# Optimization experiments

Measured on AMD Instinct MI355X. Metric: run time of the kernel, lower is better.

## Reference

```python
import jax, jax.numpy as jnp
import numpy as np

N = 8192          # number of nodes
E = 524288        # number of edges (avg degree 64)
D = 256           # latent_dim
NEG_FILL = -1e9   # torch.full fill value


def setup_inputs() -> dict:
    key = jax.random.key(0)
    k1, k2, k3, k4, k5, k6 = jax.random.split(key, 6)
    encoded = jax.random.normal(k1, (N, D), dtype=jnp.float32)
    h = jax.random.normal(k2, (N, D), dtype=jnp.float32)
    edge_index = jax.random.randint(k3, (2, E), 0, N, dtype=jnp.int64)
    edge_attr = jax.random.normal(k4, (E,), dtype=jnp.float32)
    # Linear weights (bias=False); stored as [in, out] for x @ W
    W1 = jax.random.normal(k5, (2 * D + 1, D), dtype=jnp.float32) * (1.0 / np.sqrt(2 * D + 1))
    W2 = jax.random.normal(k6, (D, 1), dtype=jnp.float32) * (1.0 / np.sqrt(D))
    return {"encoded": encoded, "h": h, "edge_index": edge_index,
            "edge_attr": edge_attr, "W1": W1, "W2": W2}


def reference(encoded, h, edge_index, edge_attr, W1, W2):
    left, right = edge_index[0], edge_index[1]
    # gather endpoint states and concat with scalar edge feature -> [E, 2D+1]
    feats = jnp.concatenate([h[left], h[right], edge_attr[:, None]], axis=1)
    # 2-layer MLP (no bias): Linear -> ReLU -> Linear -> [E]
    scores = (jax.nn.relu(feats @ W1) @ W2)[:, 0]
    # scatter into dense (N, N) matrix prefilled with -1e9
    result = jnp.full((h.shape[0], h.shape[0]), NEG_FILL, dtype=h.dtype)
    return result.at[left, right].set(scores)
```

## Files before the change

kernel.cpp:

```cpp
#include <hip/hip_runtime.h>

#define N_NODES 8192
#define E_EDGES 524288
#define D_DIM   256
#define NEG_FILL -1e9f

#define PROJ_BLOCKS 256
#define ROWS_PER_BLOCK 32
#define FILL_BLOCKS 1792

#define EDGE_BLOCKS 2048
#define EDGES_PER_WAVE 64

typedef float vfloat4 __attribute__((ext_vector_type(4)));
typedef float vfloat2 __attribute__((ext_vector_type(2)));

__global__ __launch_bounds__(256) void fill_proj_kernel(
    const float* __restrict__ h,
    const float* __restrict__ W1,
    float* __restrict__ out,
    unsigned char* __restrict__ AB)
{
    if (blockIdx.x < PROJ_BLOCKS) {
        __shared__ float hs[ROWS_PER_BLOCK * D_DIM];
        const int t  = threadIdx.x;
        const int r0 = blockIdx.x * ROWS_PER_BLOCK;
        const float* hp = h + (long long)r0 * D_DIM;
        for (int i = t; i < ROWS_PER_BLOCK * D_DIM; i += 256) hs[i] = hp[i];
        __syncthreads();

        float accA[ROWS_PER_BLOCK];
        float accB[ROWS_PER_BLOCK];
        #pragma unroll
        for (int r = 0; r < ROWS_PER_BLOCK; ++r) { accA[r] = 0.f; accB[r] = 0.f; }

        for (int k = 0; k < D_DIM; k += 4) {
            float wa0 = W1[(k + 0) * D_DIM + t];
            float wa1 = W1[(k + 1) * D_DIM + t];
            float wa2 = W1[(k + 2) * D_DIM + t];
            float wa3 = W1[(k + 3) * D_DIM + t];
            float wb0 = W1[(256 + k + 0) * D_DIM + t];
            float wb1 = W1[(256 + k + 1) * D_DIM + t];
            float wb2 = W1[(256 + k + 2) * D_DIM + t];
            float wb3 = W1[(256 + k + 3) * D_DIM + t];
            #pragma unroll
            for (int r = 0; r < ROWS_PER_BLOCK; ++r) {
                const float4 hv = *(const float4*)&hs[r * D_DIM + k];
                accA[r] = fmaf(hv.x, wa0, accA[r]);
                accA[r] = fmaf(hv.y, wa1, accA[r]);
                accA[r] = fmaf(hv.z, wa2, accA[r]);
                accA[r] = fmaf(hv.w, wa3, accA[r]);
                accB[r] = fmaf(hv.x, wb0, accB[r]);
                accB[r] = fmaf(hv.y, wb1, accB[r]);
                accB[r] = fmaf(hv.z, wb2, accB[r]);
                accB[r] = fmaf(hv.w, wb3, accB[r]);
            }
        }

        unsigned char* A = AB;
        unsigned char* B = AB + (long long)N_NODES * D_DIM;
        #pragma unroll
        for (int r = 0; r < ROWS_PER_BLOCK; ++r) {
            int pa = __builtin_amdgcn_cvt_pk_fp8_f32(accA[r], accA[r], 0, false);
            int pb = __builtin_amdgcn_cvt_pk_fp8_f32(accB[r], accB[r], 0, false);
            A[(long long)(r0 + r) * D_DIM + t] = (unsigned char)(pa & 0xFF);
            B[(long long)(r0 + r) * D_DIM + t] = (unsigned char)(pb & 0xFF);
        }
    } else {
        const int b = blockIdx.x - PROJ_BLOCKS;
        const int nvec = (N_NODES / 4) * N_NODES;
        vfloat4 fv = { NEG_FILL, NEG_FILL, NEG_FILL, NEG_FILL };
        vfloat4* o4 = (vfloat4*)out;
        for (int i = b * 256 + threadIdx.x; i < nvec; i += FILL_BLOCKS * 256)
            __builtin_nontemporal_store(fv, &o4[i]);
    }
}

__global__ __launch_bounds__(256) void edge_kernel(
    const int* __restrict__ eidx,
    const float* __restrict__ eattr,
    const float* __restrict__ W1,
    const float* __restrict__ W2,
    const unsigned char* __restrict__ AB,
    float* __restrict__ out)
{
    const int wave = blockIdx.x * 4 + (threadIdx.x >> 6);
    const int lane = threadIdx.x & 63;
    const int g    = lane >> 4;
    const int t    = lane & 15;
    const int base = wave * EDGES_PER_WAVE;

    const int   l_all = eidx[base + lane];
    const int   r_all = eidx[E_EDGES + base + lane];
    const float a_all = eattr[base + lane];

    const int j0 = t * 16;
    const float4 wl0 = *(const float4*)&W1[512 * D_DIM + j0 + 0];
    const float4 wl1 = *(const float4*)&W1[512 * D_DIM + j0 + 4];
    const float4 wl2 = *(const float4*)&W1[512 * D_DIM + j0 + 8];
    const float4 wl3 = *(const float4*)&W1[512 * D_DIM + j0 + 12];
    const float4 w20 = *(const float4*)&W2[j0 + 0];
    const float4 w21 = *(const float4*)&W2[j0 + 4];
    const float4 w22 = *(const float4*)&W2[j0 + 8];
    const float4 w23 = *(const float4*)&W2[j0 + 12];
    const unsigned char* Bt = AB + (long long)N_NODES * D_DIM;

    int   l_c  = __shfl(l_all, g);
    int   r_c  = __shfl(r_all, g);
    float at_c = __shfl(a_all, g);
    uint4 av_c = *(const uint4*)(AB + (unsigned)l_c * D_DIM + j0);
    uint4 bv_c = *(const uint4*)(Bt + (unsigned)r_c * D_DIM + j0);

    #pragma unroll 4
    for (int i = 0; i < EDGES_PER_WAVE / 4; ++i) {
        const int   l_cur = l_c;
        const int   r_cur = r_c;
        const float attr  = at_c;
        const uint4 av    = av_c;
        const uint4 bv    = bv_c;
        if (i + 1 < EDGES_PER_WAVE / 4) {
            l_c  = __shfl(l_all, 4 * (i + 1) + g);
            r_c  = __shfl(r_all, 4 * (i + 1) + g);
            at_c = __shfl(a_all, 4 * (i + 1) + g);
            av_c = *(const uint4*)(AB + (unsigned)l_c * D_DIM + j0);
            bv_c = *(const uint4*)(Bt + (unsigned)r_c * D_DIM + j0);
        }

        float s = 0.f;
        #define MLP_STEP(AV, BV, WL, W2V) {                                        \
            vfloat2 alo = __builtin_amdgcn_cvt_pk_f32_fp8((int)(AV), false);       \
            vfloat2 ahi = __builtin_amdgcn_cvt_pk_f32_fp8((int)(AV), true);        \
            vfloat2 blo = __builtin_amdgcn_cvt_pk_f32_fp8((int)(BV), false);       \
            vfloat2 bhi = __builtin_amdgcn_cvt_pk_f32_fp8((int)(BV), true);        \
            float hv;                                                              \
            hv = fmaf(attr, WL.x, alo.x + blo.x); hv = fmaxf(hv, 0.f); s = fmaf(hv, W2V.x, s); \
            hv = fmaf(attr, WL.y, alo.y + blo.y); hv = fmaxf(hv, 0.f); s = fmaf(hv, W2V.y, s); \
            hv = fmaf(attr, WL.z, ahi.x + bhi.x); hv = fmaxf(hv, 0.f); s = fmaf(hv, W2V.z, s); \
            hv = fmaf(attr, WL.w, ahi.y + bhi.y); hv = fmaxf(hv, 0.f); s = fmaf(hv, W2V.w, s); \
        }
        MLP_STEP(av.x, bv.x, wl0, w20);
        MLP_STEP(av.y, bv.y, wl1, w21);
        MLP_STEP(av.z, bv.z, wl2, w22);
        MLP_STEP(av.w, bv.w, wl3, w23);
        #undef MLP_STEP

        s += __shfl_xor(s, 8);
        s += __shfl_xor(s, 4);
        s += __shfl_xor(s, 2);
        s += __shfl_xor(s, 1);

        if (t == 0)
            __builtin_nontemporal_store(
                s, &out[(long long)l_cur * N_NODES + r_cur]);
    }
}

extern "C" void kernel_launch(void* const* d_in, const int* in_sizes, int n_in,
                              void* d_out, int out_size, void* d_ws, size_t ws_size,
                              hipStream_t stream) {
    const float* h     = (const float*)d_in[1];
    const int*   eidx  = (const int*)d_in[2];
    const float* eattr = (const float*)d_in[3];
    const float* W1    = (const float*)d_in[4];
    const float* W2    = (const float*)d_in[5];
    float* out = (float*)d_out;
    unsigned char* AB = (unsigned char*)d_ws;

    fill_proj_kernel<<<PROJ_BLOCKS + FILL_BLOCKS, 256, 0, stream>>>(h, W1, out, AB);
    edge_kernel<<<EDGE_BLOCKS, 256, 0, stream>>>(eidx, eattr, W1, W2, AB, out);
}
```

Baseline: 387.3 us.

## Pack edge indices, vectorize edge MLP with packed float2, drop LDS staging

```diff
diff --git a/kernel.cpp b/kernel.cpp
--- a/kernel.cpp
+++ b/kernel.cpp
@@ -22,12 +22,8 @@
     unsigned char* __restrict__ AB)
 {
     if (blockIdx.x < PROJ_BLOCKS) {
-        __shared__ float hs[ROWS_PER_BLOCK * D_DIM];
         const int t  = threadIdx.x;
         const int r0 = blockIdx.x * ROWS_PER_BLOCK;
-        const float* hp = h + (long long)r0 * D_DIM;
-        for (int i = t; i < ROWS_PER_BLOCK * D_DIM; i += 256) hs[i] = hp[i];
-        __syncthreads();
 
         float accA[ROWS_PER_BLOCK];
         float accB[ROWS_PER_BLOCK];
@@ -45,7 +41,7 @@
             float wb3 = W1[(256 + k + 3) * D_DIM + t];
             #pragma unroll
             for (int r = 0; r < ROWS_PER_BLOCK; ++r) {
-                const float4 hv = *(const float4*)&hs[r * D_DIM + k];
+                const float4 hv = *(const float4*)&h[(r0 + r) * D_DIM + k];
                 accA[r] = fmaf(hv.x, wa0, accA[r]);
                 accA[r] = fmaf(hv.y, wa1, accA[r]);
                 accA[r] = fmaf(hv.z, wa2, accA[r]);
@@ -90,68 +86,66 @@
     const int t    = lane & 15;
     const int base = wave * EDGES_PER_WAVE;
 
-    const int   l_all = eidx[base + lane];
-    const int   r_all = eidx[E_EDGES + base + lane];
-    const float a_all = eattr[base + lane];
+    const int   l_all = __builtin_nontemporal_load(&eidx[base + lane]);
+    const int   r_all = __builtin_nontemporal_load(&eidx[E_EDGES + base + lane]);
+    const float a_all = __builtin_nontemporal_load(&eattr[base + lane]);
+    const int   lr_all = (l_all << 13) | r_all;
 
     const int j0 = t * 16;
-    const float4 wl0 = *(const float4*)&W1[512 * D_DIM + j0 + 0];
-    const float4 wl1 = *(const float4*)&W1[512 * D_DIM + j0 + 4];
-    const float4 wl2 = *(const float4*)&W1[512 * D_DIM + j0 + 8];
-    const float4 wl3 = *(const float4*)&W1[512 * D_DIM + j0 + 12];
-    const float4 w20 = *(const float4*)&W2[j0 + 0];
-    const float4 w21 = *(const float4*)&W2[j0 + 4];
-    const float4 w22 = *(const float4*)&W2[j0 + 8];
-    const float4 w23 = *(const float4*)&W2[j0 + 12];
+    vfloat2 wl[8], w2[8];
+    const vfloat2* wlp = (const vfloat2*)&W1[512 * D_DIM + j0];
+    const vfloat2* w2p = (const vfloat2*)&W2[j0];
+    #pragma unroll
+    for (int i = 0; i < 8; ++i) { wl[i] = wlp[i]; w2[i] = w2p[i]; }
     const unsigned char* Bt = AB + (long long)N_NODES * D_DIM;
+    const vfloat2 zero2 = { 0.f, 0.f };
 
-    int   l_c  = __shfl(l_all, g);
-    int   r_c  = __shfl(r_all, g);
+    int   lr_c = __shfl(lr_all, g);
     float at_c = __shfl(a_all, g);
-    uint4 av_c = *(const uint4*)(AB + (unsigned)l_c * D_DIM + j0);
-    uint4 bv_c = *(const uint4*)(Bt + (unsigned)r_c * D_DIM + j0);
+    uint4 av_c = *(const uint4*)(AB + (unsigned)(lr_c >> 13) * D_DIM + j0);
+    uint4 bv_c = *(const uint4*)(Bt + (unsigned)(lr_c & 8191) * D_DIM + j0);
 
     #pragma unroll 4
     for (int i = 0; i < EDGES_PER_WAVE / 4; ++i) {
-        const int   l_cur = l_c;
-        const int   r_cur = r_c;
-        const float attr  = at_c;
-        const uint4 av    = av_c;
-        const uint4 bv    = bv_c;
+        const int   lr_cur = lr_c;
+        const float attr   = at_c;
+        const uint4 av     = av_c;
+        const uint4 bv     = bv_c;
         if (i + 1 < EDGES_PER_WAVE / 4) {
-            l_c  = __shfl(l_all, 4 * (i + 1) + g);
-            r_c  = __shfl(r_all, 4 * (i + 1) + g);
+            lr_c = __shfl(lr_all, 4 * (i + 1) + g);
             at_c = __shfl(a_all, 4 * (i + 1) + g);
-            av_c = *(const uint4*)(AB + (unsigned)l_c * D_DIM + j0);
-            bv_c = *(const uint4*)(Bt + (unsigned)r_c * D_DIM + j0);
+            av_c = *(const uint4*)(AB + (unsigned)(lr_c >> 13) * D_DIM + j0);
+            bv_c = *(const uint4*)(Bt + (unsigned)(lr_c & 8191) * D_DIM + j0);
         }
 
-        float s = 0.f;
-        #define MLP_STEP(AV, BV, WL, W2V) {                                        \
+        const vfloat2 attr2 = { attr, attr };
+        vfloat2 s2 = zero2;
+        #define MLP_STEP(AV, BV, WL01, WL23, W201, W223) {                         \
             vfloat2 alo = __builtin_amdgcn_cvt_pk_f32_fp8((int)(AV), false);       \
             vfloat2 ahi = __builtin_amdgcn_cvt_pk_f32_fp8((int)(AV), true);        \
             vfloat2 blo = __builtin_amdgcn_cvt_pk_f32_fp8((int)(BV), false);       \
             vfloat2 bhi = __builtin_amdgcn_cvt_pk_f32_fp8((int)(BV), true);        \
-            float hv;                                                              \
-            hv = fmaf(attr, WL.x, alo.x + blo.x); hv = fmaxf(hv, 0.f); s = fmaf(hv, W2V.x, s); \
-            hv = fmaf(attr, WL.y, alo.y + blo.y); hv = fmaxf(hv, 0.f); s = fmaf(hv, W2V.y, s); \
-            hv = fmaf(attr, WL.z, ahi.x + bhi.x); hv = fmaxf(hv, 0.f); s = fmaf(hv, W2V.z, s); \
-            hv = fmaf(attr, WL.w, ahi.y + bhi.y); hv = fmaxf(hv, 0.f); s = fmaf(hv, W2V.w, s); \
+            vfloat2 h01 = __builtin_elementwise_fma(attr2, WL01, alo + blo);       \
+            h01 = __builtin_elementwise_max(h01, zero2);                           \
+            s2  = __builtin_elementwise_fma(h01, W201, s2);                        \
+            vfloat2 h23 = __builtin_elementwise_fma(attr2, WL23, ahi + bhi);       \
+            h23 = __builtin_elementwise_max(h23, zero2);                           \
+            s2  = __builtin_elementwise_fma(h23, W223, s2);                        \
         }
-        MLP_STEP(av.x, bv.x, wl0, w20);
-        MLP_STEP(av.y, bv.y, wl1, w21);
-        MLP_STEP(av.z, bv.z, wl2, w22);
-        MLP_STEP(av.w, bv.w, wl3, w23);
+        MLP_STEP(av.x, bv.x, wl[0], wl[1], w2[0], w2[1]);
+        MLP_STEP(av.y, bv.y, wl[2], wl[3], w2[2], w2[3]);
+        MLP_STEP(av.z, bv.z, wl[4], wl[5], w2[4], w2[5]);
+        MLP_STEP(av.w, bv.w, wl[6], wl[7], w2[6], w2[7]);
         #undef MLP_STEP
 
+        float s = s2.x + s2.y;
         s += __shfl_xor(s, 8);
         s += __shfl_xor(s, 4);
         s += __shfl_xor(s, 2);
         s += __shfl_xor(s, 1);
 
         if (t == 0)
-            __builtin_nontemporal_store(
-                s, &out[(long long)l_cur * N_NODES + r_cur]);
+            __builtin_nontemporal_store(s, &out[(unsigned)lr_cur]);
     }
 }
 
```

Result: slower. 431.8 us (+11.5%).
